# Kernel tuning notes

Hardware: AMD Instinct MI355X
Metric: run time of the kernel (lower is better)

The kernel has to match this reference:

```python
import jax, jax.numpy as jnp
from jax import lax
import numpy as np
import math

D_STATE = 2
D_CONV = 4

def _ln(x, g, b, eps=1e-5):
    m = x.mean(-1, keepdims=True)
    v = ((x - m) ** 2).mean(-1, keepdims=True)
    return (x - m) * lax.rsqrt(v + eps) * g + b

def _mamba(x, Win, convw, convb, Wx, Wdt, bdt, Alog, Dp, Wout):
    # x: (b, L, d_model); expand=1 so d_inner == d_model
    b, L, dm = x.shape
    di = Win.shape[0] // 2
    n = Alog.shape[1]
    dtr = Wdt.shape[1]
    k = convw.shape[-1]
    xz = x @ Win.T                                   # (b, L, 2*di)
    xi, z = xz[..., :di], xz[..., di:]
    # causal depthwise conv1d along the sequence axis (pad left k-1, truncate to L)
    xc = jnp.pad(xi, ((0, 0), (k - 1, 0), (0, 0))).transpose(0, 2, 1)  # (b, di, L+k-1)
    xc = lax.conv_general_dilated(xc, convw, (1,), 'VALID',
                                  dimension_numbers=('NCH', 'OIH', 'NCH'),
                                  feature_group_count=di)
    xi = jax.nn.silu(xc.transpose(0, 2, 1) + convb)  # (b, L, di)
    dbl = xi @ Wx.T                                  # (b, L, dtr + 2n)
    dt = jax.nn.softplus(dbl[..., :dtr] @ Wdt.T + bdt)   # (b, L, di)
    Bm = dbl[..., dtr:dtr + n]                       # (b, L, n)
    Cm = dbl[..., dtr + n:]                          # (b, L, n)
    A = -jnp.exp(Alog)                               # (di, n)
    dA = jnp.exp(dt[..., None] * A)                  # (b, L, di, n)
    dBx = dt[..., None] * Bm[:, :, None, :] * xi[..., None]  # (b, L, di, n)

    def step(h, inp):
        dA_t, dBx_t, C_t = inp
        h = dA_t * h + dBx_t                         # (b, di, n)
        return h, jnp.einsum('bdn,bn->bd', h, C_t)

    h0 = jnp.zeros((b, di, n), x.dtype)
    _, ys = lax.scan(step, h0, (dA.transpose(1, 0, 2, 3),
                                dBx.transpose(1, 0, 2, 3),
                                Cm.transpose(1, 0, 2)))
    y = ys.transpose(1, 0, 2) + Dp * xi              # (b, L, di)
    y = y * jax.nn.silu(z)
    return y @ Wout.T                                # (b, L, out_c)

def setup_inputs():
    key = jax.random.key(0)
    ks = jax.random.split(key, 32)
    B, C, H, W = 16, 256, 32, 32
    dm = H * W
    di = dm                      # expand = 1
    dtr = math.ceil(dm / 16)     # dt_rank = 64
    n, k = D_STATE, D_CONV

    def rn(i, shape, s):
        return (jax.random.normal(ks[i], shape) * s).astype(jnp.float32)

    inp = {'x': rn(0, (B, C, H, W), 1.0)}

    def mamba_p(pfx, base):
        inp[pfx + 'Win'] = rn(base, (2 * di, dm), dm ** -0.5)
        inp[pfx + 'convw'] = rn(base + 1, (di, 1, k), k ** -0.5)
        inp[pfx + 'convb'] = jnp.zeros((di,), jnp.float32)
        inp[pfx + 'Wx'] = rn(base + 2, (dtr + 2 * n, di), di ** -0.5)
        inp[pfx + 'Wdt'] = rn(base + 3, (di, dtr), dtr ** -0.5)
        inp[pfx + 'bdt'] = rn(base + 4, (di,), 0.1)
        inp[pfx + 'Alog'] = jnp.log(jnp.broadcast_to(
            jnp.arange(1, n + 1, dtype=jnp.float32), (di, n)))
        inp[pfx + 'D'] = jnp.ones((di,), jnp.float32)
        inp[pfx + 'Wout'] = rn(base + 5, (dm, di), di ** -0.5)  # out_c = sp_dim2^2 = dm

    mamba_p('m1_', 1)
    mamba_p('m2_', 8)
    inp['ln1_g'] = jnp.ones((dm,), jnp.float32)
    inp['ln1_b'] = jnp.zeros((dm,), jnp.float32)
    inp['ln2_g'] = jnp.ones((dm,), jnp.float32)
    inp['ln2_b'] = jnp.zeros((dm,), jnp.float32)
    inp['W_mid'] = rn(15, (C, C), C ** -0.5)   # Linear_Layer inside LIFM_SPA (bias=False)
    inp['W_spa'] = rn(16, (dm, dm), dm ** -0.5)  # linear_spa (nn.Linear default bias)
    inp['b_spa'] = jnp.zeros((dm,), jnp.float32)
    inp['W_res'] = rn(17, (C, C), C ** -0.5)   # lin_chan in residual path (bias=False)
    return inp

def reference(x, m1_Win, m1_convw, m1_convb, m1_Wx, m1_Wdt, m1_bdt, m1_Alog, m1_D, m1_Wout,
              m2_Win, m2_convw, m2_convb, m2_Wx, m2_Wdt, m2_bdt, m2_Alog, m2_D, m2_Wout,
              ln1_g, ln1_b, ln2_g, ln2_b, W_mid, W_spa, b_spa, W_res):
    b, c, h, w = x.shape
    hw = h * w
    # LIFM_SPA path: SSM_spa -> Linear_Layer (channel mix + SiLU) -> SSM_spa
    s = _mamba(x.reshape(b, c, hw), m1_Win, m1_convw, m1_convb,
               m1_Wx, m1_Wdt, m1_bdt, m1_Alog, m1_D, m1_Wout)
    s = _ln(s, ln1_g, ln1_b)                               # (b, c, hw)
    s = jax.nn.silu(jnp.einsum('bcs,oc->bos', s, W_mid))   # channel linear, SiLU (dropout off in eval)
    s = _mamba(s, m2_Win, m2_convw, m2_convb,
               m2_Wx, m2_Wdt, m2_bdt, m2_Alog, m2_D, m2_Wout)
    s = _ln(s, ln2_g, ln2_b)                               # (b, out_c, hw)
    # residual path: spatial linear (+bias) + SiLU, then channel linear + SiLU
    r = jax.nn.silu(x.reshape(b, c, hw) @ W_spa.T + b_spa)
    r = jax.nn.silu(jnp.einsum('bcs,oc->bos', r, W_res))
    return jax.nn.silu(s + r).reshape(b, -1, h, w)
```

## Files before the change

### kernel.cpp

```cpp
#include <hip/hip_runtime.h>
#include <math.h>

#define BATCH 16
#define LSEQ  256
#define DM    1024
#define DI    1024
#define NROWS (BATCH*LSEQ)
#define DTR   64
#define TWO_DI 2048
#define NCH   16
#define CHL   16

typedef __attribute__((ext_vector_type(8))) short short8;
typedef __attribute__((ext_vector_type(4))) float floatx4;

__device__ __forceinline__ float siluf(float x) {
    return x / (1.0f + __expf(-x));
}
__device__ __forceinline__ float softplusf(float x) {
    return fmaxf(x, 0.0f) + log1pf(__expf(-fabsf(x)));
}
__device__ __forceinline__ unsigned short f2bf(float f) {
    unsigned int u = __float_as_uint(f);
    u += 0x7fffu + ((u >> 16) & 1u);
    return (unsigned short)(u >> 16);
}
__device__ __forceinline__ float bf2f(unsigned short s) {
    return __uint_as_float(((unsigned int)s) << 16);
}
__device__ __forceinline__ void async16(const short* g, short* l) {
    __builtin_amdgcn_global_load_lds(
        (const __attribute__((address_space(1))) unsigned int*)g,
        (__attribute__((address_space(3))) unsigned int*)l,
        16, 0, 0);
}

__global__ __launch_bounds__(256) void cast_bf16(
    const float* __restrict__ in, unsigned short* __restrict__ out)
{
    const size_t i = ((size_t)blockIdx.x * 256 + threadIdx.x) * 4;
    const float4 v = *(const float4*)(in + i);
    union { unsigned short s[4]; unsigned long long u; } p;
    p.s[0] = f2bf(v.x); p.s[1] = f2bf(v.y);
    p.s[2] = f2bf(v.z); p.s[3] = f2bf(v.w);
    *(unsigned long long*)(out + i) = p.u;
}

template <int EP, int OUT16, int BATW>
__global__ __launch_bounds__(256) void gemm_bf16_nt(
    const short* __restrict__ A,
    const short* __restrict__ W,
    const float* __restrict__ bias,
    void* __restrict__ Cout,
    int M, int N, int K)
{
    __shared__ short As[2 * 64 * 32];
    __shared__ short Bs[2 * 128 * 32];

    const int bz = BATW ? blockIdx.z : 0;
    const short* Wb = W + (size_t)bz * N * K;
    const size_t cbase = (size_t)bz * M * N;

    const int tid  = threadIdx.x;
    const int wave = tid >> 6;
    const int lane = tid & 63;
    const int wm = wave >> 1;
    const int wn = wave & 1;
    const int row0 = blockIdx.y * 64;
    const int col0 = blockIdx.x * 128;

    const int srow  = tid >> 2;
    const int skoff = (tid & 3) * 8;
    const short* gA  = A  + (size_t)(row0 + srow) * K + skoff;
    const short* gB0 = Wb + (size_t)(col0 + srow) * K + skoff;
    const short* gB1 = Wb + (size_t)(col0 + 64 + srow) * K + skoff;
    short* lA  = As + srow * 32 + skoff;
    short* lB0 = Bs + srow * 32 + skoff;
    short* lB1 = lB0 + 64 * 32;

    const int fr = lane & 15;
    const int fk = (lane >> 4) * 8;

    floatx4 acc[2][4] = {};

    async16(gA, lA);
    async16(gB0, lB0);
    async16(gB1, lB1);
    __syncthreads();

    int cur = 0;
    for (int k0 = 0; k0 < K; k0 += 32) {
        short8 af[2], bfr[4];
        const short* Ac = As + cur * 64 * 32;
        const short* Bc = Bs + cur * 128 * 32;
        #pragma unroll
        for (int i = 0; i < 2; i++)
            af[i] = *(const short8*)&Ac[(wm * 32 + i * 16 + fr) * 32 + fk];
        #pragma unroll
        for (int j = 0; j < 4; j++)
            bfr[j] = *(const short8*)&Bc[(wn * 64 + j * 16 + fr) * 32 + fk];

        if (k0 + 32 < K) {
            const int nb = (cur ^ 1);
            async16(gA + k0 + 32,  lA  + nb * 64 * 32);
            async16(gB0 + k0 + 32, lB0 + nb * 128 * 32);
            async16(gB1 + k0 + 32, lB1 + nb * 128 * 32);
        }

        #pragma unroll
        for (int i = 0; i < 2; i++)
            #pragma unroll
            for (int j = 0; j < 4; j++)
                acc[i][j] = __builtin_amdgcn_mfma_f32_16x16x32_bf16(
                    af[i], bfr[j], acc[i][j], 0, 0, 0);
        __syncthreads();
        cur ^= 1;
    }

    const int crow = row0 + wm * 32 + (lane >> 4) * 4;
    const int ccol = col0 + wn * 64 + (lane & 15);
    #pragma unroll
    for (int i = 0; i < 2; i++) {
        #pragma unroll
        for (int j = 0; j < 4; j++) {
            const int c = ccol + j * 16;
            #pragma unroll
            for (int r = 0; r < 4; r++) {
                float v = acc[i][j][r];
                if (EP == 1) v = softplusf(v + bias[c]);
                else if (EP == 2) v = siluf(v + bias[c]);
                else if (EP == 3) v = siluf(v);
                const size_t idx = cbase + (size_t)(crow + i * 16 + r) * N + c;
                if (OUT16) ((unsigned short*)Cout)[idx] = f2bf(v);
                else       ((float*)Cout)[idx] = v;
            }
        }
    }
}

__global__ __launch_bounds__(256) void gemm_nn_wcomb(
    const float* __restrict__ Wdt,
    const float* __restrict__ Wx,
    unsigned short* __restrict__ C16)
{
    __shared__ float Asf[16][64];
    __shared__ float Bsf[16][64];

    const int tid = threadIdx.x;
    const int tx = tid & 15;
    const int ty = tid >> 4;
    const int row0 = blockIdx.y * 64;
    const int col0 = blockIdx.x * 64;
    const int lrow = tid >> 2;
    const int lcol = (tid & 3) * 4;
    const int bk = tid >> 4;
    const int bn = (tid & 15) * 4;

    float acc[4][4] = {};

    for (int k0 = 0; k0 < 64; k0 += 16) {
        const float4 av = *(const float4*)(Wdt + (size_t)(row0 + lrow) * 64 + k0 + lcol);
        Asf[lcol + 0][lrow] = av.x;
        Asf[lcol + 1][lrow] = av.y;
        Asf[lcol + 2][lrow] = av.z;
        Asf[lcol + 3][lrow] = av.w;
        *(float4*)&Bsf[bk][bn] = *(const float4*)(Wx + (size_t)(k0 + bk) * 1024 + col0 + bn);
        __syncthreads();

        #pragma unroll
        for (int kk = 0; kk < 16; kk++) {
            const float4 a = *(const float4*)&Asf[kk][ty * 4];
            const float4 b = *(const float4*)&Bsf[kk][tx * 4];
            const float af[4] = {a.x, a.y, a.z, a.w};
            const float bfv[4] = {b.x, b.y, b.z, b.w};
            #pragma unroll
            for (int i = 0; i < 4; i++)
                #pragma unroll
                for (int j = 0; j < 4; j++)
                    acc[i][j] = fmaf(af[i], bfv[j], acc[i][j]);
        }
        __syncthreads();
    }

    #pragma unroll
    for (int i = 0; i < 4; i++) {
        const int r = row0 + ty * 4 + i;
        #pragma unroll
        for (int j = 0; j < 4; j++)
            C16[(size_t)r * 1024 + col0 + tx * 4 + j] = f2bf(acc[i][j]);
    }
}

__global__ __launch_bounds__(256) void conv_silu_bc(
    const float* __restrict__ xz,
    const float* __restrict__ convw,
    const float* __restrict__ convb,
    const float* __restrict__ Wx,
    unsigned short* __restrict__ xi16,
    float* __restrict__ bc)
{
    __shared__ float redc[4][4];
    const int r = blockIdx.x;
    const int l = r & (LSEQ - 1);
    const int tid = threadIdx.x;
    float p0 = 0.f, p1 = 0.f, p2 = 0.f, p3 = 0.f;
    #pragma unroll
    for (int i = 0; i < 4; i++) {
        const int d = tid + i * 256;
        const float w0 = convw[d * 4 + 0];
        const float w1 = convw[d * 4 + 1];
        const float w2 = convw[d * 4 + 2];
        const float w3 = convw[d * 4 + 3];
        float acc = w3 * xz[(size_t)r * TWO_DI + d];
        if (l >= 1) acc = fmaf(w2, xz[(size_t)(r - 1) * TWO_DI + d], acc);
        if (l >= 2) acc = fmaf(w1, xz[(size_t)(r - 2) * TWO_DI + d], acc);
        if (l >= 3) acc = fmaf(w0, xz[(size_t)(r - 3) * TWO_DI + d], acc);
        const float v = siluf(acc + convb[d]);
        xi16[(size_t)r * DI + d] = f2bf(v);
        p0 = fmaf(v, Wx[64 * 1024 + d], p0);
        p1 = fmaf(v, Wx[65 * 1024 + d], p1);
        p2 = fmaf(v, Wx[66 * 1024 + d], p2);
        p3 = fmaf(v, Wx[67 * 1024 + d], p3);
    }
    #pragma unroll
    for (int o = 32; o; o >>= 1) {
        p0 += __shfl_down(p0, o, 64);
        p1 += __shfl_down(p1, o, 64);
        p2 += __shfl_down(p2, o, 64);
        p3 += __shfl_down(p3, o, 64);
    }
    const int w = tid >> 6, lane = tid & 63;
    if (lane == 0) {
        redc[w][0] = p0; redc[w][1] = p1; redc[w][2] = p2; redc[w][3] = p3;
    }
    __syncthreads();
    if (tid < 4)
        bc[r * 4 + tid] = redc[0][tid] + redc[1][tid] + redc[2][tid] + redc[3][tid];
}

__global__ __launch_bounds__(256) void scan_part1(
    const unsigned short* __restrict__ dt16,
    const unsigned short* __restrict__ xi16,
    const float* __restrict__ bc,
    const float* __restrict__ Alog,
    float4* __restrict__ hc)
{
    const int d  = blockIdx.x * 256 + threadIdx.x;
    const int b  = blockIdx.y;
    const int ch = blockIdx.z;
    const float A0 = -__expf(Alog[d * 2 + 0]);
    const float A1 = -__expf(Alog[d * 2 + 1]);
    float h0 = 0.f, h1 = 0.f, p0 = 1.f, p1 = 1.f;
    const int r0 = b * LSEQ + ch * CHL;
    #pragma unroll 4
    for (int l = 0; l < CHL; l++) {
        const int r = r0 + l;
        const float dtv = bf2f(dt16[(size_t)r * DI + d]);
        const float xiv = bf2f(xi16[(size_t)r * DI + d]);
        const float4 bcv = *(const float4*)(bc + r * 4);
        const float e0 = __expf(dtv * A0);
        const float e1 = __expf(dtv * A1);
        const float dbx = dtv * xiv;
        h0 = fmaf(e0, h0, dbx * bcv.x);
        h1 = fmaf(e1, h1, dbx * bcv.y);
        p0 *= e0; p1 *= e1;
    }
    hc[(size_t)(b * NCH + ch) * DI + d] = make_float4(h0, h1, p0, p1);
}

__global__ __launch_bounds__(256) void scan_carry(
    const float4* __restrict__ hc,
    float2* __restrict__ ci)
{
    const int d = blockIdx.x * 256 + threadIdx.x;
    const int b = blockIdx.y;
    float c0 = 0.f, c1 = 0.f;
    #pragma unroll
    for (int ch = 0; ch < NCH; ch++) {
        const size_t idx = (size_t)(b * NCH + ch) * DI + d;
        const float4 v = hc[idx];
        ci[idx] = make_float2(c0, c1);
        c0 = fmaf(v.z, c0, v.x);
        c1 = fmaf(v.w, c1, v.y);
    }
}

__global__ __launch_bounds__(256) void scan_part2(
    const unsigned short* __restrict__ dt16,
    const unsigned short* __restrict__ xi16,
    const float* __restrict__ xz,
    const float* __restrict__ bc,
    const float* __restrict__ Alog,
    const float* __restrict__ Dp,
    const float2* __restrict__ ci,
    unsigned short* __restrict__ yg16)
{
    const int d  = blockIdx.x * 256 + threadIdx.x;
    const int b  = blockIdx.y;
    const int ch = blockIdx.z;
    const float A0 = -__expf(Alog[d * 2 + 0]);
    const float A1 = -__expf(Alog[d * 2 + 1]);
    const float Dv = Dp[d];
    const float2 c = ci[(size_t)(b * NCH + ch) * DI + d];
    float h0 = c.x, h1 = c.y;
    const int r0 = b * LSEQ + ch * CHL;
    #pragma unroll 4
    for (int l = 0; l < CHL; l++) {
        const int r = r0 + l;
        const float dtv = bf2f(dt16[(size_t)r * DI + d]);
        const float xiv = bf2f(xi16[(size_t)r * DI + d]);
        const float4 bcv = *(const float4*)(bc + r * 4);
        const float zv = xz[(size_t)r * TWO_DI + DI + d];
        const float e0 = __expf(dtv * A0);
        const float e1 = __expf(dtv * A1);
        const float dbx = dtv * xiv;
        h0 = fmaf(e0, h0, dbx * bcv.x);
        h1 = fmaf(e1, h1, dbx * bcv.y);
        const float y = fmaf(h0, bcv.z, fmaf(h1, bcv.w, Dv * xiv));
        yg16[(size_t)r * DI + d] = f2bf(y * siluf(zv));
    }
}

__global__ __launch_bounds__(256) void ln_kernel(
    float* __restrict__ s,
    const float* __restrict__ g,
    const float* __restrict__ bb)
{
    __shared__ float red[8];
    const size_t base = (size_t)blockIdx.x * DM;
    const int t = threadIdx.x;
    float x0 = s[base + t];
    float x1 = s[base + t + 256];
    float x2 = s[base + t + 512];
    float x3 = s[base + t + 768];
    float sum = x0 + x1 + x2 + x3;
    #pragma unroll
    for (int o = 32; o; o >>= 1) sum += __shfl_down(sum, o, 64);
    const int w = t >> 6, lane = t & 63;
    if (lane == 0) red[w] = sum;
    __syncthreads();
    const float m = (red[0] + red[1] + red[2] + red[3]) * (1.0f / 1024.0f);
    const float d0 = x0 - m, d1 = x1 - m, d2 = x2 - m, d3 = x3 - m;
    float ss = d0 * d0 + d1 * d1 + d2 * d2 + d3 * d3;
    #pragma unroll
    for (int o = 32; o; o >>= 1) ss += __shfl_down(ss, o, 64);
    if (lane == 0) red[4 + w] = ss;
    __syncthreads();
    const float var = (red[4] + red[5] + red[6] + red[7]) * (1.0f / 1024.0f);
    const float inv = rsqrtf(var + 1e-5f);
    s[base + t]       = d0 * inv * g[t]       + bb[t];
    s[base + t + 256] = d1 * inv * g[t + 256] + bb[t + 256];
    s[base + t + 512] = d2 * inv * g[t + 512] + bb[t + 512];
    s[base + t + 768] = d3 * inv * g[t + 768] + bb[t + 768];
}

__global__ __launch_bounds__(256) void transpose_cast(
    const float* __restrict__ in, unsigned short* __restrict__ out)
{
    __shared__ float tile[32][33];
    const int b = blockIdx.z;
    const int c0 = blockIdx.y * 32;
    const int s0 = blockIdx.x * 32;
    const int tx = threadIdx.x & 31;
    const int ty = threadIdx.x >> 5;
    const size_t ib = (size_t)b * 256 * 1024;
    const size_t ob = (size_t)b * 1024 * 256;
    #pragma unroll
    for (int i = 0; i < 4; i++)
        tile[tx][ty + i * 8] = in[ib + (size_t)(c0 + ty + i * 8) * 1024 + s0 + tx];
    __syncthreads();
    #pragma unroll
    for (int i = 0; i < 4; i++)
        out[ob + (size_t)(s0 + ty + i * 8) * 256 + c0 + tx] = f2bf(tile[ty + i * 8][tx]);
}

__global__ __launch_bounds__(256) void final_silu(
    const float* __restrict__ s, float* __restrict__ out)
{
    const size_t i = (size_t)blockIdx.x * 256 + threadIdx.x;
    out[i] = siluf(s[i] + out[i]);
}

extern "C" void kernel_launch(void* const* d_in, const int* in_sizes, int n_in,
                              void* d_out, int out_size, void* d_ws, size_t ws_size,
                              hipStream_t stream)
{
    const float* x        = (const float*)d_in[0];
    const float* m1_Win   = (const float*)d_in[1];
    const float* m1_convw = (const float*)d_in[2];
    const float* m1_convb = (const float*)d_in[3];
    const float* m1_Wx    = (const float*)d_in[4];
    const float* m1_Wdt   = (const float*)d_in[5];
    const float* m1_bdt   = (const float*)d_in[6];
    const float* m1_Alog  = (const float*)d_in[7];
    const float* m1_D     = (const float*)d_in[8];
    const float* m1_Wout  = (const float*)d_in[9];
    const float* m2_Win   = (const float*)d_in[10];
    const float* m2_convw = (const float*)d_in[11];
    const float* m2_convb = (const float*)d_in[12];
    const float* m2_Wx    = (const float*)d_in[13];
    const float* m2_Wdt   = (const float*)d_in[14];
    const float* m2_bdt   = (const float*)d_in[15];
    const float* m2_Alog  = (const float*)d_in[16];
    const float* m2_D     = (const float*)d_in[17];
    const float* m2_Wout  = (const float*)d_in[18];
    const float* ln1_g    = (const float*)d_in[19];
    const float* ln1_b    = (const float*)d_in[20];
    const float* ln2_g    = (const float*)d_in[21];
    const float* ln2_b    = (const float*)d_in[22];
    const float* W_mid    = (const float*)d_in[23];
    const float* W_spa    = (const float*)d_in[24];
    const float* b_spa    = (const float*)d_in[25];
    const float* W_res    = (const float*)d_in[26];

    float* ws = (float*)d_ws;
    size_t off = 0;
    float* buf_xz  = ws + off; off += (size_t)NROWS * TWO_DI;
    float* buf_s   = ws + off; off += (size_t)NROWS * DI;
    float* buf_bc  = ws + off; off += (size_t)NROWS * 4;
    float4* buf_hc = (float4*)(ws + off); off += (size_t)BATCH * NCH * DI * 4;
    float2* buf_ci = (float2*)(ws + off); off += (size_t)BATCH * NCH * DI * 2;
    unsigned short* bx     = (unsigned short*)(ws + off); off += (size_t)NROWS * DI / 2;
    unsigned short* xi16   = (unsigned short*)(ws + off); off += (size_t)NROWS * DI / 2;
    unsigned short* yg16   = (unsigned short*)(ws + off); off += (size_t)NROWS * DI / 2;
    unsigned short* sT16   = (unsigned short*)(ws + off); off += (size_t)NROWS * DI / 2;
    unsigned short* dt16   = (unsigned short*)(ws + off); off += (size_t)NROWS * DI / 2;
    unsigned short* win16  = (unsigned short*)(ws + off); off += (size_t)TWO_DI * DM / 2;
    unsigned short* wout16 = (unsigned short*)(ws + off); off += (size_t)DM * DI / 2;
    unsigned short* wspa16 = (unsigned short*)(ws + off); off += (size_t)DM * DM / 2;
    unsigned short* wcomb16= (unsigned short*)(ws + off); off += (size_t)DI * DI / 2;
    unsigned short* wmid16 = (unsigned short*)(ws + off); off += (size_t)LSEQ * LSEQ / 2;
    unsigned short* wres16 = (unsigned short*)(ws + off); off += (size_t)LSEQ * LSEQ / 2;
    unsigned short* t16 = yg16;
    float* buf_res = buf_xz;
    unsigned short* rT16 = sT16;
    (void)ws_size; (void)n_in; (void)in_sizes; (void)out_size;

    const dim3 blk(256);

    auto mamba = [&](const unsigned short* inp16, const float* Win,
                     const float* convw, const float* convb, const float* Wx,
                     const float* Wdt, const float* bdt, const float* Alog,
                     const float* Dp, const float* Wout, float* out_buf) {
        cast_bf16<<<dim3((TWO_DI * DM) / 1024), blk, 0, stream>>>(Win, win16);
        cast_bf16<<<dim3((DM * DI) / 1024), blk, 0, stream>>>(Wout, wout16);
        gemm_nn_wcomb<<<dim3(16, 16), blk, 0, stream>>>(Wdt, Wx, wcomb16);
        gemm_bf16_nt<0, 0, 0><<<dim3(TWO_DI / 128, NROWS / 64), blk, 0, stream>>>(
            (const short*)inp16, (const short*)win16, nullptr, buf_xz,
            NROWS, TWO_DI, DM);
        conv_silu_bc<<<dim3(NROWS), blk, 0, stream>>>(
            buf_xz, convw, convb, Wx, xi16, buf_bc);
        gemm_bf16_nt<1, 1, 0><<<dim3(DI / 128, NROWS / 64), blk, 0, stream>>>(
            (const short*)xi16, (const short*)wcomb16, bdt, dt16,
            NROWS, DI, DI);
        scan_part1<<<dim3(DI / 256, BATCH, NCH), blk, 0, stream>>>(
            dt16, xi16, buf_bc, Alog, buf_hc);
        scan_carry<<<dim3(DI / 256, BATCH), blk, 0, stream>>>(buf_hc, buf_ci);
        scan_part2<<<dim3(DI / 256, BATCH, NCH), blk, 0, stream>>>(
            dt16, xi16, buf_xz, buf_bc, Alog, Dp, buf_ci, yg16);
        gemm_bf16_nt<0, 0, 0><<<dim3(DM / 128, NROWS / 64), blk, 0, stream>>>(
            (const short*)yg16, (const short*)wout16, nullptr, out_buf,
            NROWS, DM, DI);
    };

    cast_bf16<<<dim3((NROWS * DM) / 1024), blk, 0, stream>>>(x, bx);
    cast_bf16<<<dim3((DM * DM) / 1024), blk, 0, stream>>>(W_spa, wspa16);
    cast_bf16<<<dim3((LSEQ * LSEQ) / 1024), blk, 0, stream>>>(W_mid, wmid16);
    cast_bf16<<<dim3((LSEQ * LSEQ) / 1024), blk, 0, stream>>>(W_res, wres16);

    mamba(bx, m1_Win, m1_convw, m1_convb, m1_Wx, m1_Wdt, m1_bdt, m1_Alog, m1_D,
          m1_Wout, buf_s);
    ln_kernel<<<dim3(NROWS), blk, 0, stream>>>(buf_s, ln1_g, ln1_b);

    transpose_cast<<<dim3(32, 8, BATCH), blk, 0, stream>>>(buf_s, sT16);
    gemm_bf16_nt<3, 1, 1><<<dim3(DM / 128, LSEQ / 64, BATCH), blk, 0, stream>>>(
        (const short*)wmid16, (const short*)sT16, nullptr, (void*)t16,
        LSEQ, DM, LSEQ);

    mamba(t16, m2_Win, m2_convw, m2_convb, m2_Wx, m2_Wdt, m2_bdt, m2_Alog,
          m2_D, m2_Wout, buf_s);
    ln_kernel<<<dim3(NROWS), blk, 0, stream>>>(buf_s, ln2_g, ln2_b);

    gemm_bf16_nt<2, 0, 0><<<dim3(DM / 128, NROWS / 64), blk, 0, stream>>>(
        (const short*)bx, (const short*)wspa16, b_spa, buf_res,
        NROWS, DM, DM);
    transpose_cast<<<dim3(32, 8, BATCH), blk, 0, stream>>>(buf_res, rT16);
    gemm_bf16_nt<3, 0, 1><<<dim3(DM / 128, LSEQ / 64, BATCH), blk, 0, stream>>>(
        (const short*)wres16, (const short*)rT16, nullptr, d_out,
        LSEQ, DM, LSEQ);

    final_silu<<<dim3((NROWS * DM) / 256), blk, 0, stream>>>(
        buf_s, (float*)d_out);
}
```

Baseline: 459.7 us.

## Use single-wave GEMM tiles, bf16 intermediates, merged casts, fused final SiLU

Replaces the 4-wave 64x128 GEMM with a single-wave 64x64 tile kernel. The xz and residual intermediates are now stored in bf16 instead of fp32. All weight and input casts are merged into one launch, and both wcomb products are computed in one launch. The final residual add and SiLU are fused into the last GEMM's epilogue. This reduces launch count and memory traffic, but the one-wave blocks give lower per-CU occupancy, and storing xz in bf16 adds rounding error.

```diff
diff --git a/kernel.cpp b/kernel.cpp
--- a/kernel.cpp
+++ b/kernel.cpp
@@ -13,6 +13,7 @@
 
 typedef __attribute__((ext_vector_type(8))) short short8;
 typedef __attribute__((ext_vector_type(4))) float floatx4;
+typedef __attribute__((ext_vector_type(4))) unsigned short ushortx4;
 
 __device__ __forceinline__ float siluf(float x) {
     return x / (1.0f + __expf(-x));
@@ -35,10 +36,27 @@
         16, 0, 0);
 }
 
-__global__ __launch_bounds__(256) void cast_bf16(
-    const float* __restrict__ in, unsigned short* __restrict__ out)
-{
-    const size_t i = ((size_t)blockIdx.x * 256 + threadIdx.x) * 4;
+__global__ __launch_bounds__(256) void cast8(
+    const float* __restrict__ x,    unsigned short* __restrict__ ox,
+    const float* __restrict__ w1i,  unsigned short* __restrict__ o1i,
+    const float* __restrict__ w1o,  unsigned short* __restrict__ o1o,
+    const float* __restrict__ w2i,  unsigned short* __restrict__ o2i,
+    const float* __restrict__ w2o,  unsigned short* __restrict__ o2o,
+    const float* __restrict__ wsp,  unsigned short* __restrict__ osp,
+    const float* __restrict__ wmd,  unsigned short* __restrict__ omd,
+    const float* __restrict__ wrs,  unsigned short* __restrict__ ors)
+{
+    const int b = blockIdx.x;
+    const float* in; unsigned short* out; int base;
+    if      (b <  4096) { in = x;   out = ox;  base = 0; }
+    else if (b <  6144) { in = w1i; out = o1i; base = 4096; }
+    else if (b <  7168) { in = w1o; out = o1o; base = 6144; }
+    else if (b <  9216) { in = w2i; out = o2i; base = 7168; }
+    else if (b < 10240) { in = w2o; out = o2o; base = 9216; }
+    else if (b < 11264) { in = wsp; out = osp; base = 10240; }
+    else if (b < 11328) { in = wmd; out = omd; base = 11264; }
+    else                { in = wrs; out = ors; base = 11328; }
+    const size_t i = ((size_t)(b - base) * 256 + threadIdx.x) * 4;
     const float4 v = *(const float4*)(in + i);
     union { unsigned short s[4]; unsigned long long u; } p;
     p.s[0] = f2bf(v.x); p.s[1] = f2bf(v.y);
@@ -46,69 +64,65 @@
     *(unsigned long long*)(out + i) = p.u;
 }
 
-template <int EP, int OUT16, int BATW>
-__global__ __launch_bounds__(256) void gemm_bf16_nt(
+template <int EP, int OUT16, int BATW, int FIN>
+__global__ __launch_bounds__(64) void gemm1w(
     const short* __restrict__ A,
     const short* __restrict__ W,
     const float* __restrict__ bias,
+    const float* __restrict__ Sadd,
     void* __restrict__ Cout,
     int M, int N, int K)
 {
     __shared__ short As[2 * 64 * 32];
-    __shared__ short Bs[2 * 128 * 32];
+    __shared__ short Bs[2 * 64 * 32];
 
     const int bz = BATW ? blockIdx.z : 0;
     const short* Wb = W + (size_t)bz * N * K;
     const size_t cbase = (size_t)bz * M * N;
 
-    const int tid  = threadIdx.x;
-    const int wave = tid >> 6;
-    const int lane = tid & 63;
-    const int wm = wave >> 1;
-    const int wn = wave & 1;
+    const int lane = threadIdx.x;
     const int row0 = blockIdx.y * 64;
-    const int col0 = blockIdx.x * 128;
-
-    const int srow  = tid >> 2;
-    const int skoff = (tid & 3) * 8;
-    const short* gA  = A  + (size_t)(row0 + srow) * K + skoff;
-    const short* gB0 = Wb + (size_t)(col0 + srow) * K + skoff;
-    const short* gB1 = Wb + (size_t)(col0 + 64 + srow) * K + skoff;
-    short* lA  = As + srow * 32 + skoff;
-    short* lB0 = Bs + srow * 32 + skoff;
-    short* lB1 = lB0 + 64 * 32;
+    const int col0 = blockIdx.x * 64;
+
+    const int srow  = lane >> 2;
+    const int skoff = (lane & 3) * 8;
+    const short* gA = A  + (size_t)(row0 + srow) * K + skoff;
+    const short* gB = Wb + (size_t)(col0 + srow) * K + skoff;
+    short* lA = As + srow * 32 + skoff;
+    short* lB = Bs + srow * 32 + skoff;
 
     const int fr = lane & 15;
     const int fk = (lane >> 4) * 8;
 
-    floatx4 acc[2][4] = {};
-
-    async16(gA, lA);
-    async16(gB0, lB0);
-    async16(gB1, lB1);
+    floatx4 acc[4][4] = {};
+
+    #pragma unroll
+    for (int r = 0; r < 4; r++) {
+        async16(gA + (size_t)(r * 16) * K, lA + r * 16 * 32);
+        async16(gB + (size_t)(r * 16) * K, lB + r * 16 * 32);
+    }
     __syncthreads();
 
     int cur = 0;
     for (int k0 = 0; k0 < K; k0 += 32) {
-        short8 af[2], bfr[4];
         const short* Ac = As + cur * 64 * 32;
-        const short* Bc = Bs + cur * 128 * 32;
+        const short* Bc = Bs + cur * 64 * 32;
+        short8 af[4], bfr[4];
         #pragma unroll
-        for (int i = 0; i < 2; i++)
-            af[i] = *(const short8*)&Ac[(wm * 32 + i * 16 + fr) * 32 + fk];
+        for (int t = 0; t < 4; t++) {
+            af[t]  = *(const short8*)&Ac[(t * 16 + fr) * 32 + fk];
+            bfr[t] = *(const short8*)&Bc[(t * 16 + fr) * 32 + fk];
+        }
+        if (k0 + 32 < K) {
+            const int nb = cur ^ 1;
+            #pragma unroll
+            for (int r = 0; r < 4; r++) {
+                async16(gA + (size_t)(r * 16) * K + k0 + 32, lA + (nb * 64 + r * 16) * 32);
+                async16(gB + (size_t)(r * 16) * K + k0 + 32, lB + (nb * 64 + r * 16) * 32);
+            }
+        }
         #pragma unroll
-        for (int j = 0; j < 4; j++)
-            bfr[j] = *(const short8*)&Bc[(wn * 64 + j * 16 + fr) * 32 + fk];
-
-        if (k0 + 32 < K) {
-            const int nb = (cur ^ 1);
-            async16(gA + k0 + 32,  lA  + nb * 64 * 32);
-            async16(gB0 + k0 + 32, lB0 + nb * 128 * 32);
-            async16(gB1 + k0 + 32, lB1 + nb * 128 * 32);
-        }
-
-        #pragma unroll
-        for (int i = 0; i < 2; i++)
+        for (int i = 0; i < 4; i++)
             #pragma unroll
             for (int j = 0; j < 4; j++)
                 acc[i][j] = __builtin_amdgcn_mfma_f32_16x16x32_bf16(
@@ -117,10 +131,10 @@
         cur ^= 1;
     }
 
-    const int crow = row0 + wm * 32 + (lane >> 4) * 4;
-    const int ccol = col0 + wn * 64 + (lane & 15);
-    #pragma unroll
-    for (int i = 0; i < 2; i++) {
+    const int crow = row0 + (lane >> 4) * 4;
+    const int ccol = col0 + (lane & 15);
+    #pragma unroll
+    for (int i = 0; i < 4; i++) {
         #pragma unroll
         for (int j = 0; j < 4; j++) {
             const int c = ccol + j * 16;
@@ -131,6 +145,7 @@
                 else if (EP == 2) v = siluf(v + bias[c]);
                 else if (EP == 3) v = siluf(v);
                 const size_t idx = cbase + (size_t)(crow + i * 16 + r) * N + c;
+                if (FIN) v = siluf(Sadd[idx] + v);
                 if (OUT16) ((unsigned short*)Cout)[idx] = f2bf(v);
                 else       ((float*)Cout)[idx] = v;
             }
@@ -139,10 +154,15 @@
 }
 
 __global__ __launch_bounds__(256) void gemm_nn_wcomb(
-    const float* __restrict__ Wdt,
-    const float* __restrict__ Wx,
-    unsigned short* __restrict__ C16)
-{
+    const float* __restrict__ Wdt1, const float* __restrict__ Wx1,
+    unsigned short* __restrict__ C1,
+    const float* __restrict__ Wdt2, const float* __restrict__ Wx2,
+    unsigned short* __restrict__ C2)
+{
+    const float* Wdt = blockIdx.z ? Wdt2 : Wdt1;
+    const float* Wx  = blockIdx.z ? Wx2  : Wx1;
+    unsigned short* C16 = blockIdx.z ? C2 : C1;
+
     __shared__ float Asf[16][64];
     __shared__ float Bsf[16][64];
 
@@ -192,7 +212,7 @@
 }
 
 __global__ __launch_bounds__(256) void conv_silu_bc(
-    const float* __restrict__ xz,
+    const unsigned short* __restrict__ xz16,
     const float* __restrict__ convw,
     const float* __restrict__ convb,
     const float* __restrict__ Wx,
@@ -203,25 +223,33 @@
     const int r = blockIdx.x;
     const int l = r & (LSEQ - 1);
     const int tid = threadIdx.x;
+    const int d0 = tid * 4;
+
+    ushortx4 x0 = *(const ushortx4*)(xz16 + (size_t)r * TWO_DI + d0);
+    ushortx4 x1 = {0,0,0,0}, x2 = {0,0,0,0}, x3 = {0,0,0,0};
+    if (l >= 1) x1 = *(const ushortx4*)(xz16 + (size_t)(r - 1) * TWO_DI + d0);
+    if (l >= 2) x2 = *(const ushortx4*)(xz16 + (size_t)(r - 2) * TWO_DI + d0);
+    if (l >= 3) x3 = *(const ushortx4*)(xz16 + (size_t)(r - 3) * TWO_DI + d0);
+
     float p0 = 0.f, p1 = 0.f, p2 = 0.f, p3 = 0.f;
-    #pragma unroll
-    for (int i = 0; i < 4; i++) {
-        const int d = tid + i * 256;
-        const float w0 = convw[d * 4 + 0];
-        const float w1 = convw[d * 4 + 1];
-        const float w2 = convw[d * 4 + 2];
-        const float w3 = convw[d * 4 + 3];
-        float acc = w3 * xz[(size_t)r * TWO_DI + d];
-        if (l >= 1) acc = fmaf(w2, xz[(size_t)(r - 1) * TWO_DI + d], acc);
-        if (l >= 2) acc = fmaf(w1, xz[(size_t)(r - 2) * TWO_DI + d], acc);
-        if (l >= 3) acc = fmaf(w0, xz[(size_t)(r - 3) * TWO_DI + d], acc);
+    ushortx4 outv;
+    #pragma unroll
+    for (int j = 0; j < 4; j++) {
+        const int d = d0 + j;
+        const float4 w = *(const float4*)(convw + d * 4);
+        float acc = w.w * bf2f(x0[j]);
+        acc = fmaf(w.z, bf2f(x1[j]), acc);
+        acc = fmaf(w.y, bf2f(x2[j]), acc);
+        acc = fmaf(w.x, bf2f(x3[j]), acc);
         const float v = siluf(acc + convb[d]);
-        xi16[(size_t)r * DI + d] = f2bf(v);
+        outv[j] = f2bf(v);
         p0 = fmaf(v, Wx[64 * 1024 + d], p0);
         p1 = fmaf(v, Wx[65 * 1024 + d], p1);
         p2 = fmaf(v, Wx[66 * 1024 + d], p2);
         p3 = fmaf(v, Wx[67 * 1024 + d], p3);
     }
+    *(ushortx4*)(xi16 + (size_t)r * DI + d0) = outv;
+
     #pragma unroll
     for (int o = 32; o; o >>= 1) {
         p0 += __shfl_down(p0, o, 64);
@@ -288,7 +316,7 @@
 __global__ __launch_bounds__(256) void scan_part2(
     const unsigned short* __restrict__ dt16,
     const unsigned short* __restrict__ xi16,
-    const float* __restrict__ xz,
+    const unsigned short* __restrict__ xz16,
     const float* __restrict__ bc,
     const float* __restrict__ Alog,
     const float* __restrict__ Dp,
@@ -310,7 +338,7 @@
         const float dtv = bf2f(dt16[(size_t)r * DI + d]);
         const float xiv = bf2f(xi16[(size_t)r * DI + d]);
         const float4 bcv = *(const float4*)(bc + r * 4);
-        const float zv = xz[(size_t)r * TWO_DI + DI + d];
+        const float zv = bf2f(xz16[(size_t)r * TWO_DI + DI + d]);
         const float e0 = __expf(dtv * A0);
         const float e1 = __expf(dtv * A1);
         const float dbx = dtv * xiv;
@@ -374,11 +402,24 @@
         out[ob + (size_t)(s0 + ty + i * 8) * 256 + c0 + tx] = f2bf(tile[ty + i * 8][tx]);
 }
 
-__global__ __launch_bounds__(256) void final_silu(
-    const float* __restrict__ s, float* __restrict__ out)
-{
-    const size_t i = (size_t)blockIdx.x * 256 + threadIdx.x;
-    out[i] = siluf(s[i] + out[i]);
+__global__ __launch_bounds__(256) void transpose16(
+    const unsigned short* __restrict__ in, unsigned short* __restrict__ out)
+{
+    __shared__ unsigned short tile[32][34];
+    const int b = blockIdx.z;
+    const int c0 = blockIdx.y * 32;
+    const int s0 = blockIdx.x * 32;
+    const int tx = threadIdx.x & 31;
+    const int ty = threadIdx.x >> 5;
+    const size_t ib = (size_t)b * 256 * 1024;
+    const size_t ob = (size_t)b * 1024 * 256;
+    #pragma unroll
+    for (int i = 0; i < 4; i++)
+        tile[tx][ty + i * 8] = in[ib + (size_t)(c0 + ty + i * 8) * 1024 + s0 + tx];
+    __syncthreads();
+    #pragma unroll
+    for (int i = 0; i < 4; i++)
+        out[ob + (size_t)(s0 + ty + i * 8) * 256 + c0 + tx] = tile[ty + i * 8][tx];
 }
 
 extern "C" void kernel_launch(void* const* d_in, const int* in_sizes, int n_in,
@@ -415,80 +456,80 @@
 
     float* ws = (float*)d_ws;
     size_t off = 0;
-    float* buf_xz  = ws + off; off += (size_t)NROWS * TWO_DI;
     float* buf_s   = ws + off; off += (size_t)NROWS * DI;
     float* buf_bc  = ws + off; off += (size_t)NROWS * 4;
     float4* buf_hc = (float4*)(ws + off); off += (size_t)BATCH * NCH * DI * 4;
     float2* buf_ci = (float2*)(ws + off); off += (size_t)BATCH * NCH * DI * 2;
+    unsigned short* xz16   = (unsigned short*)(ws + off); off += (size_t)NROWS * TWO_DI / 2;
     unsigned short* bx     = (unsigned short*)(ws + off); off += (size_t)NROWS * DI / 2;
     unsigned short* xi16   = (unsigned short*)(ws + off); off += (size_t)NROWS * DI / 2;
     unsigned short* yg16   = (unsigned short*)(ws + off); off += (size_t)NROWS * DI / 2;
     unsigned short* sT16   = (unsigned short*)(ws + off); off += (size_t)NROWS * DI / 2;
     unsigned short* dt16   = (unsigned short*)(ws + off); off += (size_t)NROWS * DI / 2;
-    unsigned short* win16  = (unsigned short*)(ws + off); off += (size_t)TWO_DI * DM / 2;
-    unsigned short* wout16 = (unsigned short*)(ws + off); off += (size_t)DM * DI / 2;
+    unsigned short* res16  = (unsigned short*)(ws + off); off += (size_t)NROWS * DI / 2;
+    unsigned short* win1   = (unsigned short*)(ws + off); off += (size_t)TWO_DI * DM / 2;
+    unsigned short* wout1  = (unsigned short*)(ws + off); off += (size_t)DM * DI / 2;
+    unsigned short* win2   = (unsigned short*)(ws + off); off += (size_t)TWO_DI * DM / 2;
+    unsigned short* wout2  = (unsigned short*)(ws + off); off += (size_t)DM * DI / 2;
     unsigned short* wspa16 = (unsigned short*)(ws + off); off += (size_t)DM * DM / 2;
-    unsigned short* wcomb16= (unsigned short*)(ws + off); off += (size_t)DI * DI / 2;
+    unsigned short* wcomb1 = (unsigned short*)(ws + off); off += (size_t)DI * DI / 2;
+    unsigned short* wcomb2 = (unsigned short*)(ws + off); off += (size_t)DI * DI / 2;
     unsigned short* wmid16 = (unsigned short*)(ws + off); off += (size_t)LSEQ * LSEQ / 2;
     unsigned short* wres16 = (unsigned short*)(ws + off); off += (size_t)LSEQ * LSEQ / 2;
-    unsigned short* t16 = yg16;
-    float* buf_res = buf_xz;
+    unsigned short* t16  = yg16;
     unsigned short* rT16 = sT16;
     (void)ws_size; (void)n_in; (void)in_sizes; (void)out_size;
 
     const dim3 blk(256);
-
-    auto mamba = [&](const unsigned short* inp16, const float* Win,
+    const dim3 blk64(64);
+
+    cast8<<<dim3(11392), blk, 0, stream>>>(
+        x, bx, m1_Win, win1, m1_Wout, wout1, m2_Win, win2, m2_Wout, wout2,
+        W_spa, wspa16, W_mid, wmid16, W_res, wres16);
+    gemm_nn_wcomb<<<dim3(16, 16, 2), blk, 0, stream>>>(
+        m1_Wdt, m1_Wx, wcomb1, m2_Wdt, m2_Wx, wcomb2);
+
+    auto mamba = [&](const unsigned short* inp16, const unsigned short* win16,
+                     const unsigned short* wcomb16, const unsigned short* wout16,
                      const float* convw, const float* convb, const float* Wx,
-                     const float* Wdt, const float* bdt, const float* Alog,
-                     const float* Dp, const float* Wout, float* out_buf) {
-        cast_bf16<<<dim3((TWO_DI * DM) / 1024), blk, 0, stream>>>(Win, win16);
-        cast_bf16<<<dim3((DM * DI) / 1024), blk, 0, stream>>>(Wout, wout16);
-        gemm_nn_wcomb<<<dim3(16, 16), blk, 0, stream>>>(Wdt, Wx, wcomb16);
-        gemm_bf16_nt<0, 0, 0><<<dim3(TWO_DI / 128, NROWS / 64), blk, 0, stream>>>(
-            (const short*)inp16, (const short*)win16, nullptr, buf_xz,
-            NROWS, TWO_DI, DM);
+                     const float* bdt, const float* Alog, const float* Dp,
+                     float* out_buf) {
+        gemm1w<0, 1, 0, 0><<<dim3(TWO_DI / 64, NROWS / 64), blk64, 0, stream>>>(
+            (const short*)inp16, (const short*)win16, nullptr, nullptr,
+            (void*)xz16, NROWS, TWO_DI, DM);
         conv_silu_bc<<<dim3(NROWS), blk, 0, stream>>>(
-            buf_xz, convw, convb, Wx, xi16, buf_bc);
-        gemm_bf16_nt<1, 1, 0><<<dim3(DI / 128, NROWS / 64), blk, 0, stream>>>(
-            (const short*)xi16, (const short*)wcomb16, bdt, dt16,
-            NROWS, DI, DI);
+            xz16, convw, convb, Wx, xi16, buf_bc);
+        gemm1w<1, 1, 0, 0><<<dim3(DI / 64, NROWS / 64), blk64, 0, stream>>>(
+            (const short*)xi16, (const short*)wcomb16, bdt, nullptr,
+            (void*)dt16, NROWS, DI, DI);
         scan_part1<<<dim3(DI / 256, BATCH, NCH), blk, 0, stream>>>(
             dt16, xi16, buf_bc, Alog, buf_hc);
         scan_carry<<<dim3(DI / 256, BATCH), blk, 0, stream>>>(buf_hc, buf_ci);
         scan_part2<<<dim3(DI / 256, BATCH, NCH), blk, 0, stream>>>(
-            dt16, xi16, buf_xz, buf_bc, Alog, Dp, buf_ci, yg16);
-        gemm_bf16_nt<0, 0, 0><<<dim3(DM / 128, NROWS / 64), blk, 0, stream>>>(
-            (const short*)yg16, (const short*)wout16, nullptr, out_buf,
-            NROWS, DM, DI);
+            dt16, xi16, xz16, buf_bc, Alog, Dp, buf_ci, yg16);
+        gemm1w<0, 0, 0, 0><<<dim3(DM / 64, NROWS / 64), blk64, 0, stream>>>(
+            (const short*)yg16, (const short*)wout16, nullptr, nullptr,
+            (void*)out_buf, NROWS, DM, DI);
     };
 
-    cast_bf16<<<dim3((NROWS * DM) / 1024), blk, 0, stream>>>(x, bx);
-    cast_bf16<<<dim3((DM * DM) / 1024), blk, 0, stream>>>(W_spa, wspa16);
-    cast_bf16<<<dim3((LSEQ * LSEQ) / 1024), blk, 0, stream>>>(W_mid, wmid16);
-    cast_bf16<<<dim3((LSEQ * LSEQ) / 1024), blk, 0, stream>>>(W_res, wres16);
-
-    mamba(bx, m1_Win, m1_convw, m1_convb, m1_Wx, m1_Wdt, m1_bdt, m1_Alog, m1_D,
-          m1_Wout, buf_s);
+    mamba(bx, win1, wcomb1, wout1, m1_convw, m1_convb, m1_Wx, m1_bdt,
+          m1_Alog, m1_D, buf_s);
     ln_kernel<<<dim3(NROWS), blk, 0, stream>>>(buf_s, ln1_g, ln1_b);
 
     transpose_cast<<<dim3(32, 8, BATCH), blk, 0, stream>>>(buf_s, sT16);
-    gemm_bf16_nt<3, 1, 1><<<dim3(DM / 128, LSEQ / 64, BATCH), blk, 0, stream>>>(
-        (const short*)wmid16, (const short*)sT16, nullptr, (void*)t16,
-        LSEQ, DM, LSEQ);
-
-    mamba(t16, m2_Win, m2_convw, m2_convb, m2_Wx, m2_Wdt, m2_bdt, m2_Alog,
-          m2_D, m2_Wout, buf_s);
+    gemm1w<3, 1, 1, 0><<<dim3(DM / 64, LSEQ / 64, BATCH), blk64, 0, stream>>>(
+        (const short*)wmid16, (const short*)sT16, nullptr, nullptr,
+        (void*)t16, LSEQ, DM, LSEQ);
+
+    mamba(t16, win2, wcomb2, wout2, m2_convw, m2_convb, m2_Wx, m2_bdt,
+          m2_Alog, m2_D, buf_s);
     ln_kernel<<<dim3(NROWS), blk, 0, stream>>>(buf_s, ln2_g, ln2_b);
 
-    gemm_bf16_nt<2, 0, 0><<<dim3(DM / 128, NROWS / 64), blk, 0, stream>>>(
-        (const short*)bx, (const short*)wspa16, b_spa, buf_res,
-        NROWS, DM, DM);
-    transpose_cast<<<dim3(32, 8, BATCH), blk, 0, stream>>>(buf_res, rT16);
-    gemm_bf16_nt<3, 0, 1><<<dim3(DM / 128, LSEQ / 64, BATCH), blk, 0, stream>>>(
-        (const short*)wres16, (const short*)rT16, nullptr, d_out,
-        LSEQ, DM, LSEQ);
-
-    final_silu<<<dim3((NROWS * DM) / 256), blk, 0, stream>>>(
-        buf_s, (float*)d_out);
-}
+    gemm1w<2, 1, 0, 0><<<dim3(DM / 64, NROWS / 64), blk64, 0, stream>>>(
+        (const short*)bx, (const short*)wspa16, b_spa, nullptr,
+        (void*)res16, NROWS, DM, DM);
+    transpose16<<<dim3(32, 8, BATCH), blk, 0, stream>>>(res16, rT16);
+    gemm1w<3, 0, 1, 1><<<dim3(DM / 64, LSEQ / 64, BATCH), blk64, 0, stream>>>(
+        (const short*)wres16, (const short*)rT16, nullptr, buf_s,
+        d_out, LSEQ, DM, LSEQ);
+}
```

New measurement: 472.5 us. +2.8%, slower.
